# Optimization experiments

Hardware: AMD Instinct MI355X
Metric: run time of the kernel (lower is better)

The kernel has to match this reference:

```python
import jax, jax.numpy as jnp
import numpy as np

B, N, C, K = 2048, 64, 256, 3  # batch, num_proposals, hidden_dim, kernel_size
EPS = 1e-5


def setup_inputs() -> dict:
    key = jax.random.key(0)
    k0, k1, k2 = jax.random.split(key, 3)
    query = jax.random.normal(k0, (B, N, C), dtype=jnp.float32)
    value = jax.random.normal(k1, (B, N, C), dtype=jnp.float32)
    # weight_linear: Linear(C, N + K), trunc_normal std=0.02, zero bias
    W_lin = (jax.random.truncated_normal(k2, -2.0, 2.0, (N + K, C), dtype=jnp.float32) * 0.02)
    b_lin = jnp.zeros((N + K,), dtype=jnp.float32)
    ln_gamma = jnp.ones((C,), dtype=jnp.float32)
    ln_beta = jnp.zeros((C,), dtype=jnp.float32)
    return {"query": query, "value": value, "W_lin": W_lin, "b_lin": b_lin,
            "ln_gamma": ln_gamma, "ln_beta": ln_beta}


def reference(query, value, W_lin, b_lin, ln_gamma, ln_beta):
    # dynamic weights: [B, N, N + K]
    dyw = jnp.einsum('bnc,oc->bno', query, W_lin) + b_lin
    depth_w = dyw[..., :K]          # [B, N, K]  per-proposal depthwise kernel
    point_w = dyw[..., K:]          # [B, M, N]  out-proposal m mixes in-proposal n

    # depthwise conv1d over C with padding='same' (torch conv1d = cross-correlation)
    vpad = jnp.pad(value, ((0, 0), (0, 0), (1, 1)))                 # [B, N, C+2]
    win = jnp.stack([vpad[..., k:k + C] for k in range(K)], axis=2)  # [B, N, K, C]
    depth = jax.nn.relu(jnp.einsum('bnkc,bnk->bnc', win, depth_w))   # [B, N, C]

    # pointwise (1x1) conv mixing the N proposal channels
    point = jnp.einsum('bmn,bnc->bmc', point_w, depth)               # [B, N, C]

    # LayerNorm over last dim C
    mu = jnp.mean(point, axis=-1, keepdims=True)
    var = jnp.mean(jnp.square(point - mu), axis=-1, keepdims=True)
    out = (point - mu) * jax.lax.rsqrt(var + EPS) * ln_gamma + ln_beta
    return out
```

## Files before the change

kernel.cpp:

```cpp
#include <hip/hip_runtime.h>

#define NB 2048
#define NN 64
#define NC 256
#define EPSV 1e-5f

typedef __attribute__((ext_vector_type(8))) short bf16x8;
typedef __attribute__((ext_vector_type(4))) float f32x4;

union U8 { unsigned u[4]; unsigned long long d[2]; bf16x8 v; };

__device__ __forceinline__ unsigned f_bits(float f) {
    union { float f; unsigned u; } x; x.f = f; return x.u;
}
__device__ __forceinline__ unsigned short f2bf_r(float f) {
    return (unsigned short)((f_bits(f) + 0x8000u) >> 16);
}
__device__ __forceinline__ unsigned pack2(float a, float b) {
    return ((f_bits(a) + 0x8000u) >> 16) | ((f_bits(b) + 0x8000u) & 0xffff0000u);
}

extern "C" __global__ __launch_bounds__(256, 3)
void dysep_mfma(const float* __restrict__ q, const float* __restrict__ v,
                const float* __restrict__ W, const float* __restrict__ bl,
                const float* __restrict__ gam, const float* __restrict__ bet,
                float* __restrict__ out)
{
    __shared__ __align__(16) unsigned short sDT[256 * 66];
    __shared__ __align__(16) unsigned short sPw[64][68];
    __shared__ __align__(16) float sCw[64][4];

    const int tid = threadIdx.x;
    const int w  = tid >> 6;
    const int l  = tid & 63;
    const int lr = l & 15;
    const int lg = l >> 4;
    const long base = (long)blockIdx.x * (NN * NC);

    bf16x8 af[8];
    {
        const float* qrow = q + base + (long)(w * 16 + lr) * NC + lg * 8;
#pragma unroll
        for (int kg = 0; kg < 8; ++kg) {
            float4 a0 = *(const float4*)(qrow + kg * 32);
            float4 a1 = *(const float4*)(qrow + kg * 32 + 4);
            U8 u;
            u.u[0] = pack2(a0.x, a0.y); u.u[1] = pack2(a0.z, a0.w);
            u.u[2] = pack2(a1.x, a1.y); u.u[3] = pack2(a1.z, a1.w);
            af[kg] = u.v;
        }
    }
    f32x4 acc[5];
    {
        f32x4 zz = {0.f, 0.f, 0.f, 0.f};
#pragma unroll
        for (int nt = 0; nt < 5; ++nt) acc[nt] = zz;
    }
#pragma unroll
    for (int nt = 0; nt < 5; ++nt) {
        const int o = nt * 16 + lr;
        const int oc = (o < 67) ? o : 0;
        const float* wrow = W + (long)oc * NC + lg * 8;
#pragma unroll
        for (int kg = 0; kg < 8; ++kg) {
            float4 b0 = *(const float4*)(wrow + kg * 32);
            float4 b1 = *(const float4*)(wrow + kg * 32 + 4);
            U8 u;
            u.u[0] = pack2(b0.x, b0.y); u.u[1] = pack2(b0.z, b0.w);
            u.u[2] = pack2(b1.x, b1.y); u.u[3] = pack2(b1.z, b1.w);
            acc[nt] = __builtin_amdgcn_mfma_f32_16x16x32_bf16(af[kg], u.v, acc[nt], 0, 0, 0);
        }
    }
#pragma unroll
    for (int nt = 0; nt < 5; ++nt) {
        const int o = nt * 16 + lr;
        const float bb = (o < 67) ? bl[o] : 0.f;
#pragma unroll
        for (int r = 0; r < 4; ++r) {
            const int m = w * 16 + lg * 4 + r;
            const float val = acc[nt][r] + bb;
            if (o < 3) sCw[m][o] = val;
            else if (o < 67) sPw[m][o - 3] = f2bf_r(val);
        }
    }
    __syncthreads();

    {
#pragma unroll 4
        for (int i = 0; i < 16; ++i) {
            const int n = i * 4 + w;
            const float w0 = sCw[n][0], w1 = sCw[n][1], w2 = sCw[n][2];
            float4 vv = *(const float4*)(v + base + (long)n * NC + 4 * l);
            float prev = __shfl(vv.w, (l + 63) & 63);
            float next = __shfl(vv.x, (l + 1) & 63);
            if (l == 0) prev = 0.f;
            if (l == 63) next = 0.f;
            const float d0 = fmaxf(0.f, w0 * prev + w1 * vv.x + w2 * vv.y);
            const float d1 = fmaxf(0.f, w0 * vv.x + w1 * vv.y + w2 * vv.z);
            const float d2 = fmaxf(0.f, w0 * vv.y + w1 * vv.z + w2 * vv.w);
            const float d3 = fmaxf(0.f, w0 * vv.z + w1 * vv.w + w2 * next);
            const int c0 = 4 * l;
            sDT[(c0 + 0) * 66 + n] = f2bf_r(d0);
            sDT[(c0 + 1) * 66 + n] = f2bf_r(d1);
            sDT[(c0 + 2) * 66 + n] = f2bf_r(d2);
            sDT[(c0 + 3) * 66 + n] = f2bf_r(d3);
        }
    }
    __syncthreads();

    bf16x8 pa[2];
#pragma unroll
    for (int kg = 0; kg < 2; ++kg) {
        const unsigned long long* p =
            (const unsigned long long*)&sPw[w * 16 + lr][kg * 32 + lg * 8];
        U8 u; u.d[0] = p[0]; u.d[1] = p[1];
        pa[kg] = u.v;
    }
    f32x4 acc3[16];
    {
        f32x4 zz = {0.f, 0.f, 0.f, 0.f};
#pragma unroll
        for (int ct = 0; ct < 16; ++ct) acc3[ct] = zz;
    }
#pragma unroll
    for (int ct = 0; ct < 16; ++ct) {
#pragma unroll
        for (int kg = 0; kg < 2; ++kg) {
            const unsigned* p = (const unsigned*)&sDT[(ct * 16 + lr) * 66 + kg * 32 + lg * 8];
            U8 u; u.u[0] = p[0]; u.u[1] = p[1]; u.u[2] = p[2]; u.u[3] = p[3];
            acc3[ct] = __builtin_amdgcn_mfma_f32_16x16x32_bf16(pa[kg], u.v, acc3[ct], 0, 0, 0);
        }
    }
    float mus[4], rss[4];
#pragma unroll
    for (int r = 0; r < 4; ++r) {
        float s1 = 0.f, s2 = 0.f;
#pragma unroll
        for (int ct = 0; ct < 16; ++ct) {
            const float x = acc3[ct][r];
            s1 += x; s2 += x * x;
        }
#pragma unroll
        for (int off = 1; off < 16; off <<= 1) {
            s1 += __shfl_xor(s1, off);
            s2 += __shfl_xor(s2, off);
        }
        const float mu = s1 * (1.f / 256.f);
        const float var = s2 * (1.f / 256.f) - mu * mu;
        mus[r] = mu;
        rss[r] = rsqrtf(var + EPSV);
    }
    {
        float* orow = out + base + (long)(w * 16 + lg * 4) * NC + lr;
#pragma unroll
        for (int ct = 0; ct < 16; ++ct) {
            const float gg = gam[ct * 16 + lr];
            const float bb = bet[ct * 16 + lr];
#pragma unroll
            for (int r = 0; r < 4; ++r) {
                orow[(long)r * NC + ct * 16] =
                    (acc3[ct][r] - mus[r]) * rss[r] * gg + bb;
            }
        }
    }
}

extern "C" void kernel_launch(void* const* d_in, const int* in_sizes, int n_in,
                              void* d_out, int out_size, void* d_ws, size_t ws_size,
                              hipStream_t stream) {
    const float* q   = (const float*)d_in[0];
    const float* v   = (const float*)d_in[1];
    const float* W   = (const float*)d_in[2];
    const float* bl  = (const float*)d_in[3];
    const float* gam = (const float*)d_in[4];
    const float* bet = (const float*)d_in[5];
    float* o = (float*)d_out;
    hipLaunchKernelGGL(dysep_mfma, dim3(NB), dim3(256), 0, stream,
                       q, v, W, bl, gam, bet, o);
}
```

Before: 125.3 us.

## Prepack W into bf16 MFMA fragments and split work across 8 waves

Adds a small pre-kernel that converts W into bf16 MFMA B-fragments once per call, so the main kernel loads ready-made fragments instead of converting fp32 W in every block. The main kernel now uses 512 threads: each of the 4 M-tiles is handled by two waves, which split the output N-tiles of the weight GEMM, the depthwise rows and the C-tiles of the pointwise GEMM. LayerNorm partial sums from the two halves are combined through shared memory, which adds a barrier. The intent is more latency hiding and less redundant conversion work, at the cost of an extra launch and some imbalance (one half handles 3 N-tiles, the other 2).

```diff
diff --git a/kernel.cpp b/kernel.cpp
--- a/kernel.cpp
+++ b/kernel.cpp
@@ -20,18 +20,41 @@
     return ((f_bits(a) + 0x8000u) >> 16) | ((f_bits(b) + 0x8000u) & 0xffff0000u);
 }
 
-extern "C" __global__ __launch_bounds__(256, 3)
-void dysep_mfma(const float* __restrict__ q, const float* __restrict__ v,
-                const float* __restrict__ W, const float* __restrict__ bl,
-                const float* __restrict__ gam, const float* __restrict__ bet,
-                float* __restrict__ out)
+extern "C" __global__ void prep_wfrag(const float* __restrict__ W,
+                                      unsigned short* __restrict__ wf)
+{
+    const int idx = blockIdx.x * 256 + threadIdx.x;
+    if (idx >= 40 * 64) return;
+    const int f = idx >> 6, l = idx & 63;
+    const int nt = f >> 3, kg = f & 7;
+    const int o = nt * 16 + (l & 15);
+    const int kb = kg * 32 + (l >> 4) * 8;
+    float x[8];
+#pragma unroll
+    for (int e = 0; e < 8; ++e)
+        x[e] = (o < 67) ? W[o * NC + kb + e] : 0.f;
+    uint4 pk;
+    pk.x = pack2(x[0], x[1]); pk.y = pack2(x[2], x[3]);
+    pk.z = pack2(x[4], x[5]); pk.w = pack2(x[6], x[7]);
+    *(uint4*)(wf + (size_t)idx * 8) = pk;
+}
+
+extern "C" __global__ __launch_bounds__(512, 6)
+void dysep_mfma8(const float* __restrict__ q, const float* __restrict__ v,
+                 const unsigned short* __restrict__ wfrag,
+                 const float* __restrict__ bl,
+                 const float* __restrict__ gam, const float* __restrict__ bet,
+                 float* __restrict__ out)
 {
     __shared__ __align__(16) unsigned short sDT[256 * 66];
     __shared__ __align__(16) unsigned short sPw[64][68];
     __shared__ __align__(16) float sCw[64][4];
+    __shared__ __align__(16) float sLN[64][4];
 
     const int tid = threadIdx.x;
     const int w  = tid >> 6;
+    const int mt = w & 3;
+    const int h  = w >> 2;
     const int l  = tid & 63;
     const int lr = l & 15;
     const int lg = l >> 4;
@@ -39,7 +62,7 @@
 
     bf16x8 af[8];
     {
-        const float* qrow = q + base + (long)(w * 16 + lr) * NC + lg * 8;
+        const float* qrow = q + base + (long)(mt * 16 + lr) * NC + lg * 8;
 #pragma unroll
         for (int kg = 0; kg < 8; ++kg) {
             float4 a0 = *(const float4*)(qrow + kg * 32);
@@ -50,45 +73,46 @@
             af[kg] = u.v;
         }
     }
-    f32x4 acc[5];
+    const int ntCount = 3 - h;
+    f32x4 acc[3];
     {
         f32x4 zz = {0.f, 0.f, 0.f, 0.f};
 #pragma unroll
-        for (int nt = 0; nt < 5; ++nt) acc[nt] = zz;
-    }
-#pragma unroll
-    for (int nt = 0; nt < 5; ++nt) {
-        const int o = nt * 16 + lr;
-        const int oc = (o < 67) ? o : 0;
-        const float* wrow = W + (long)oc * NC + lg * 8;
-#pragma unroll
-        for (int kg = 0; kg < 8; ++kg) {
-            float4 b0 = *(const float4*)(wrow + kg * 32);
-            float4 b1 = *(const float4*)(wrow + kg * 32 + 4);
-            U8 u;
-            u.u[0] = pack2(b0.x, b0.y); u.u[1] = pack2(b0.z, b0.w);
-            u.u[2] = pack2(b1.x, b1.y); u.u[3] = pack2(b1.z, b1.w);
-            acc[nt] = __builtin_amdgcn_mfma_f32_16x16x32_bf16(af[kg], u.v, acc[nt], 0, 0, 0);
-        }
-    }
-#pragma unroll
-    for (int nt = 0; nt < 5; ++nt) {
-        const int o = nt * 16 + lr;
-        const float bb = (o < 67) ? bl[o] : 0.f;
-#pragma unroll
-        for (int r = 0; r < 4; ++r) {
-            const int m = w * 16 + lg * 4 + r;
-            const float val = acc[nt][r] + bb;
-            if (o < 3) sCw[m][o] = val;
-            else if (o < 67) sPw[m][o - 3] = f2bf_r(val);
+        for (int t = 0; t < 3; ++t) acc[t] = zz;
+    }
+    const U8* __restrict__ wf8 = (const U8*)wfrag;
+#pragma unroll
+    for (int t = 0; t < 3; ++t) {
+        if (t < ntCount) {
+            const int nt = h * 3 + t;
+            const U8* fr = wf8 + (nt * 8) * 64 + l;
+#pragma unroll
+            for (int kg = 0; kg < 8; ++kg) {
+                U8 u = fr[kg * 64];
+                acc[t] = __builtin_amdgcn_mfma_f32_16x16x32_bf16(af[kg], u.v, acc[t], 0, 0, 0);
+            }
+        }
+    }
+#pragma unroll
+    for (int t = 0; t < 3; ++t) {
+        if (t < ntCount) {
+            const int o = (h * 3 + t) * 16 + lr;
+            const float bb = (o < 67) ? bl[o] : 0.f;
+#pragma unroll
+            for (int r = 0; r < 4; ++r) {
+                const int m = mt * 16 + lg * 4 + r;
+                const float val = acc[t][r] + bb;
+                if (o < 3) sCw[m][o] = val;
+                else if (o < 67) sPw[m][o - 3] = f2bf_r(val);
+            }
         }
     }
     __syncthreads();
 
     {
 #pragma unroll 4
-        for (int i = 0; i < 16; ++i) {
-            const int n = i * 4 + w;
+        for (int i = 0; i < 8; ++i) {
+            const int n = i * 8 + w;
             const float w0 = sCw[n][0], w1 = sCw[n][1], w2 = sCw[n][2];
             float4 vv = *(const float4*)(v + base + (long)n * NC + 4 * l);
             float prev = __shfl(vv.w, (l + 63) & 63);
@@ -112,54 +136,76 @@
 #pragma unroll
     for (int kg = 0; kg < 2; ++kg) {
         const unsigned long long* p =
-            (const unsigned long long*)&sPw[w * 16 + lr][kg * 32 + lg * 8];
+            (const unsigned long long*)&sPw[mt * 16 + lr][kg * 32 + lg * 8];
         U8 u; u.d[0] = p[0]; u.d[1] = p[1];
         pa[kg] = u.v;
     }
-    f32x4 acc3[16];
+    f32x4 acc3[8];
     {
         f32x4 zz = {0.f, 0.f, 0.f, 0.f};
 #pragma unroll
-        for (int ct = 0; ct < 16; ++ct) acc3[ct] = zz;
-    }
-#pragma unroll
-    for (int ct = 0; ct < 16; ++ct) {
+        for (int t = 0; t < 8; ++t) acc3[t] = zz;
+    }
+#pragma unroll
+    for (int t = 0; t < 8; ++t) {
+        const int ct = h * 8 + t;
 #pragma unroll
         for (int kg = 0; kg < 2; ++kg) {
             const unsigned* p = (const unsigned*)&sDT[(ct * 16 + lr) * 66 + kg * 32 + lg * 8];
             U8 u; u.u[0] = p[0]; u.u[1] = p[1]; u.u[2] = p[2]; u.u[3] = p[3];
-            acc3[ct] = __builtin_amdgcn_mfma_f32_16x16x32_bf16(pa[kg], u.v, acc3[ct], 0, 0, 0);
-        }
-    }
+            acc3[t] = __builtin_amdgcn_mfma_f32_16x16x32_bf16(pa[kg], u.v, acc3[t], 0, 0, 0);
+        }
+    }
+    {
+        float s1a[4], s2a[4];
+#pragma unroll
+        for (int r = 0; r < 4; ++r) {
+            float s1 = 0.f, s2 = 0.f;
+#pragma unroll
+            for (int t = 0; t < 8; ++t) {
+                const float x = acc3[t][r];
+                s1 += x; s2 += x * x;
+            }
+#pragma unroll
+            for (int off = 1; off < 16; off <<= 1) {
+                s1 += __shfl_xor(s1, off);
+                s2 += __shfl_xor(s2, off);
+            }
+            s1a[r] = s1; s2a[r] = s2;
+        }
+        if (lr == 0) {
+#pragma unroll
+            for (int r = 0; r < 4; ++r) {
+                const int m = mt * 16 + lg * 4 + r;
+                sLN[m][2 * h + 0] = s1a[r];
+                sLN[m][2 * h + 1] = s2a[r];
+            }
+        }
+    }
+    __syncthreads();
+
     float mus[4], rss[4];
 #pragma unroll
     for (int r = 0; r < 4; ++r) {
-        float s1 = 0.f, s2 = 0.f;
-#pragma unroll
-        for (int ct = 0; ct < 16; ++ct) {
-            const float x = acc3[ct][r];
-            s1 += x; s2 += x * x;
-        }
-#pragma unroll
-        for (int off = 1; off < 16; off <<= 1) {
-            s1 += __shfl_xor(s1, off);
-            s2 += __shfl_xor(s2, off);
-        }
-        const float mu = s1 * (1.f / 256.f);
-        const float var = s2 * (1.f / 256.f) - mu * mu;
+        const int m = mt * 16 + lg * 4 + r;
+        const float S1 = sLN[m][0] + sLN[m][2];
+        const float S2 = sLN[m][1] + sLN[m][3];
+        const float mu = S1 * (1.f / 256.f);
+        const float var = S2 * (1.f / 256.f) - mu * mu;
         mus[r] = mu;
         rss[r] = rsqrtf(var + EPSV);
     }
     {
-        float* orow = out + base + (long)(w * 16 + lg * 4) * NC + lr;
-#pragma unroll
-        for (int ct = 0; ct < 16; ++ct) {
+        float* orow = out + base + (long)(mt * 16 + lg * 4) * NC + lr;
+#pragma unroll
+        for (int t = 0; t < 8; ++t) {
+            const int ct = h * 8 + t;
             const float gg = gam[ct * 16 + lr];
             const float bb = bet[ct * 16 + lr];
 #pragma unroll
             for (int r = 0; r < 4; ++r) {
                 orow[(long)r * NC + ct * 16] =
-                    (acc3[ct][r] - mus[r]) * rss[r] * gg + bb;
+                    (acc3[t][r] - mus[r]) * rss[r] * gg + bb;
             }
         }
     }
@@ -175,6 +221,9 @@
     const float* gam = (const float*)d_in[4];
     const float* bet = (const float*)d_in[5];
     float* o = (float*)d_out;
-    hipLaunchKernelGGL(dysep_mfma, dim3(NB), dim3(256), 0, stream,
-                       q, v, W, bl, gam, bet, o);
-}
+    unsigned short* wf = (unsigned short*)d_ws;
+
+    hipLaunchKernelGGL(prep_wfrag, dim3(10), dim3(256), 0, stream, W, wf);
+    hipLaunchKernelGGL(dysep_mfma8, dim3(NB), dim3(512), 0, stream,
+                       q, v, wf, bl, gam, bet, o);
+}
```

New measurement: 109.3 us. 12.7% less time.
